# Kernel optimization log

Measured on AMD Instinct MI355X. Metric: run time of the kernel, lower is better.

The kernel has to match this reference:

```python
import jax, jax.numpy as jnp
import numpy as np

B, S, D, H = 2, 2048, 1024, 16
DK = D // H
THETA = 10000.0


def _freqs_cos_sin(dim, seq_len, theta=THETA):
    # matches precompute_freqs_cis: freqs over full d_model, pairs of adjacent dims
    inv = 1.0 / theta ** (np.arange(0, dim, 2)[: dim // 2].astype(np.float32) / dim)
    t = np.arange(seq_len, dtype=np.float32)
    ang = np.outer(t, inv)  # [S, D/2]
    return jnp.asarray(np.cos(ang)), jnp.asarray(np.sin(ang))


def setup_inputs() -> dict:
    key = jax.random.key(0)
    ks = jax.random.split(key, 11)
    sc = 1.0 / np.sqrt(D)
    cos, sin = _freqs_cos_sin(D, S)
    return {
        "query": jax.random.normal(ks[0], (B, S, D), jnp.float32),
        "key": jax.random.normal(ks[1], (B, S, D), jnp.float32),
        "value": jax.random.normal(ks[2], (B, S, D), jnp.float32),
        "wq": jax.random.normal(ks[3], (D, D), jnp.float32) * sc,
        "bq": jnp.zeros((D,), jnp.float32),
        "wk": jax.random.normal(ks[4], (D, D), jnp.float32) * sc,
        "bk": jnp.zeros((D,), jnp.float32),
        "wv": jax.random.normal(ks[5], (D, D), jnp.float32) * sc,
        "bv": jnp.zeros((D,), jnp.float32),
        "wo": jax.random.normal(ks[6], (D, D), jnp.float32) * sc,
        "bo": jnp.zeros((D,), jnp.float32),
        "cos": cos,  # [S, D/2]
        "sin": sin,  # [S, D/2]
    }


def _rope(x, cos, sin):
    # x: [B,S,D]; pairs are adjacent elements along D (view_as_complex semantics)
    xr = x.reshape(*x.shape[:-1], -1, 2)  # [B,S,D/2,2]
    x0, x1 = xr[..., 0], xr[..., 1]
    c, s = cos[None], sin[None]  # broadcast over batch
    o0 = x0 * c - x1 * s
    o1 = x0 * s + x1 * c
    return jnp.stack([o0, o1], axis=-1).reshape(x.shape)


def reference(query, key, value, wq, bq, wk, bk, wv, bv, wo, bo, cos, sin):
    q = query @ wq.T + bq
    k = key @ wk.T + bk
    v = value @ wv.T + bv
    q = _rope(q, cos, sin)
    k = _rope(k, cos, sin)
    # split heads: [B,S,D] -> [B,H,S,DK]
    q = q.reshape(B, S, H, DK).transpose(0, 2, 1, 3)
    k = k.reshape(B, S, H, DK).transpose(0, 2, 1, 3)
    v = v.reshape(B, S, H, DK).transpose(0, 2, 1, 3)
    scores = jnp.einsum("bhqd,bhkd->bhqk", q, k) / jnp.sqrt(jnp.float32(DK))
    attn = jax.nn.softmax(scores, axis=-1)  # dropout is identity in eval
    out = jnp.einsum("bhqk,bhkd->bhqd", attn, v)
    out = out.transpose(0, 2, 1, 3).reshape(B, S, D)
    return out @ wo.T + bo
```

## Files before the change

kernel.cpp:

```cpp
#include <hip/hip_runtime.h>
#include <hip/hip_fp16.h>

typedef _Float16 f16;
using f16x8 = __attribute__((ext_vector_type(8))) _Float16;
using h2 = __attribute__((ext_vector_type(2))) __fp16;
using f32x4 = __attribute__((ext_vector_type(4))) float;
using f32x16 = __attribute__((ext_vector_type(16))) float;

#define LOG2E 1.4426950408889634f

__device__ __forceinline__ void gload16(const void* g, void* l) {
  __builtin_amdgcn_global_load_lds(
      (const __attribute__((address_space(1))) void*)g,
      (__attribute__((address_space(3))) void*)l, 16, 0, 0);
}

__device__ __forceinline__ float b32(h2 x) { return __builtin_bit_cast(float, x); }
__device__ __forceinline__ unsigned u32(h2 x) { return __builtin_bit_cast(unsigned, x); }

__global__ __launch_bounds__(256) void convert_k(
    const float* __restrict__ q, const float* __restrict__ k, const float* __restrict__ v,
    const float* __restrict__ wq, const float* __restrict__ wk,
    const float* __restrict__ wv, const float* __restrict__ wo,
    f16* __restrict__ dst) {
  const size_t SEG = (size_t)4 * 1024 * 1024;
  size_t i = ((size_t)blockIdx.x * 256 + threadIdx.x) * 8;
  const float* src; size_t off;
  if (i < SEG)            { src = q;  off = i; }
  else if (i < 2 * SEG)   { src = k;  off = i - SEG; }
  else if (i < 3 * SEG)   { src = v;  off = i - 2 * SEG; }
  else {
    size_t wi = i - 3 * SEG;
    int s = (int)(wi >> 20);
    src = (s == 0) ? wq : (s == 1) ? wk : (s == 2) ? wv : wo;
    off = wi & ((1u << 20) - 1);
  }
  float4 a = *(const float4*)(src + off);
  float4 b = *(const float4*)(src + off + 4);
  f16x8 o;
  o[0] = (f16)a.x; o[1] = (f16)a.y; o[2] = (f16)a.z; o[3] = (f16)a.w;
  o[4] = (f16)b.x; o[5] = (f16)b.y; o[6] = (f16)b.z; o[7] = (f16)b.w;
  *(f16x8*)(dst + i) = o;
}

template <int QKV>
__global__ __launch_bounds__(256) void gemm_k(
    const f16* __restrict__ Abase, const f16* __restrict__ Wbase,
    const float* __restrict__ b0, const float* __restrict__ b1, const float* __restrict__ b2,
    const float* __restrict__ cosT, const float* __restrict__ sinT,
    f16* __restrict__ qh, f16* __restrict__ kh, f16* __restrict__ vt,
    float* __restrict__ outF) {
  __shared__ f16 As[128 * 32];
  __shared__ f16 Bs[128 * 32];
  int tid = threadIdx.x, wid = tid >> 6, lane = tid & 63;
  int z = QKV ? blockIdx.z : 0;
  const f16* A = Abase + (size_t)z * (4u * 1024 * 1024);
  const f16* W = Wbase + (size_t)z * (1024u * 1024);
  int m0 = blockIdx.y * 128, n0 = blockIdx.x * 128;
  int wr = wid >> 1, wc = wid & 1;
  f32x4 acc[4][4] = {};

  for (int kt = 0; kt < 32; ++kt) {
    int k0 = kt * 32;
    __syncthreads();
#pragma unroll
    for (int p = 0; p < 2; ++p) {
      int row = p * 64 + (tid >> 2);
      int srcslot = (tid & 3) ^ (row & 3);
      gload16(A + (size_t)(m0 + row) * 1024 + k0 + srcslot * 8,
              (void*)(As + p * 2048 + wid * 512));
      gload16(W + (size_t)(n0 + row) * 1024 + k0 + srcslot * 8,
              (void*)(Bs + p * 2048 + wid * 512));
    }
    __syncthreads();
    f16x8 af[4], bf[4];
#pragma unroll
    for (int i = 0; i < 4; ++i) {
      int row = wr * 64 + i * 16 + (lane & 15);
      int slot = (lane >> 4) ^ (row & 3);
      af[i] = *(const f16x8*)(As + row * 32 + slot * 8);
    }
#pragma unroll
    for (int j = 0; j < 4; ++j) {
      int col = wc * 64 + j * 16 + (lane & 15);
      int slot = (lane >> 4) ^ (col & 3);
      bf[j] = *(const f16x8*)(Bs + col * 32 + slot * 8);
    }
#pragma unroll
    for (int i = 0; i < 4; ++i)
#pragma unroll
      for (int j = 0; j < 4; ++j)
        acc[i][j] = __builtin_amdgcn_mfma_f32_16x16x32_f16(af[i], bf[j], acc[i][j], 0, 0, 0);
  }

  const float* bias = QKV ? (z == 0 ? b0 : (z == 1 ? b1 : b2)) : b0;
#pragma unroll
  for (int i = 0; i < 4; ++i) {
#pragma unroll
    for (int j = 0; j < 4; ++j) {
#pragma unroll
      for (int r = 0; r < 4; ++r) {
        int grow = m0 + wr * 64 + i * 16 + ((lane >> 4) << 2) + r;
        int gcol = n0 + wc * 64 + j * 16 + (lane & 15);
        float val = acc[i][j][r] + bias[gcol];
        if (QKV) {
          int s = grow & 2047, bb = grow >> 11;
          int h = gcol >> 6, dk = gcol & 63;
          if (z < 2) {
            float pr = __shfl_xor(val, 1);
            int j2 = gcol >> 1;
            float c = cosT[s * 512 + j2], sn = sinT[s * 512 + j2];
            val = (lane & 1) ? (c * val + sn * pr) : (c * val - sn * pr);
            if (z == 0) val *= 0.125f * LOG2E;
            f16* dst = (z == 0) ? qh : kh;
            dst[(((size_t)bb * 16 + h) * 2048 + s) * 64 + dk] = (f16)val;
          } else {
            vt[(((size_t)bb * 16 + h) * 64 + dk) * 2048 + s] = (f16)val;
          }
        } else {
          outF[(size_t)grow * 1024 + gcol] = val;
        }
      }
    }
  }
}

__global__ __launch_bounds__(256, 4) void flash_k(
    const f16* __restrict__ qh, const f16* __restrict__ kh, const f16* __restrict__ vt,
    f16* __restrict__ op, float2* __restrict__ mlbuf) {
  __shared__ f16 Ks[2][64 * 64];
  __shared__ f16 Vs[2][64 * 64];
  int tid = threadIdx.x, wid = tid >> 6, lane = tid & 63;
  int l31 = lane & 31, hi = lane >> 5;
  int qt = blockIdx.x, h = blockIdx.y, z = blockIdx.z;
  int b = z >> 1, ks = z & 1;
  size_t bh = (size_t)b * 16 + h;
  const f16* qp = qh + bh * (2048 * 64);
  const f16* kp = kh + bh * (2048 * 64) + (size_t)ks * 1024 * 64;
  const f16* vp = vt + bh * (64 * 2048) + ks * 1024;
  int qrow = qt * 128 + wid * 32 + l31;

  f16x8 qf[4];
#pragma unroll
  for (int kk = 0; kk < 4; ++kk)
    qf[kk] = *(const f16x8*)(qp + (size_t)qrow * 64 + kk * 16 + hi * 8);

  int srowA = tid >> 3, srowB = srowA + 32;
  int schA = (tid & 7) ^ (srowA & 7);
  int schB = (tid & 7) ^ (srowB & 7);
  const f16* ksrcA = kp + (size_t)srowA * 64 + schA * 8;
  const f16* ksrcB = kp + (size_t)srowB * 64 + schB * 8;
  const f16* vsrcA = vp + (size_t)srowA * 2048 + schA * 8;
  const f16* vsrcB = vp + (size_t)srowB * 2048 + schB * 8;

  int offr[2][4];
#pragma unroll
  for (int kb = 0; kb < 2; ++kb)
#pragma unroll
    for (int kk = 0; kk < 4; ++kk) {
      int row = kb * 32 + l31;
      offr[kb][kk] = (row * 128 + kk * 32 + hi * 16) ^ ((row & 7) << 4);
    }

  float m_ = -1e30f, l_ = 0.f;
  f32x16 oacc[2] = {};

  gload16(ksrcA, (char*)&Ks[0][0] + tid * 16);
  gload16(ksrcB, (char*)&Ks[0][0] + 4096 + tid * 16);
  gload16(vsrcA, (char*)&Vs[0][0] + tid * 16);
  gload16(vsrcB, (char*)&Vs[0][0] + 4096 + tid * 16);
  __syncthreads();

  int cur = 0;
  for (int kt = 0; kt < 16; ++kt) {
    if (kt + 1 < 16) {
      gload16(ksrcA + (size_t)(kt + 1) * 4096, (char*)&Ks[cur ^ 1][0] + tid * 16);
      gload16(ksrcB + (size_t)(kt + 1) * 4096, (char*)&Ks[cur ^ 1][0] + 4096 + tid * 16);
      gload16(vsrcA + (size_t)(kt + 1) * 64, (char*)&Vs[cur ^ 1][0] + tid * 16);
      gload16(vsrcB + (size_t)(kt + 1) * 64, (char*)&Vs[cur ^ 1][0] + 4096 + tid * 16);
    }

    const char* kbase = (const char*)&Ks[cur][0];
    f32x16 sacc[2] = {};
#pragma unroll
    for (int kb = 0; kb < 2; ++kb)
#pragma unroll
      for (int kk = 0; kk < 4; ++kk) {
        f16x8 af = *(const f16x8*)(kbase + offr[kb][kk]);
        sacc[kb] = __builtin_amdgcn_mfma_f32_32x32x16_f16(af, qf[kk], sacc[kb], 0, 0, 0);
      }

    float t16[16];
#pragma unroll
    for (int i = 0; i < 16; ++i) t16[i] = fmaxf(sacc[0][i], sacc[1][i]);
#pragma unroll
    for (int s = 8; s; s >>= 1)
#pragma unroll
      for (int i = 0; i < s; ++i) t16[i] = fmaxf(t16[i], t16[i + s]);
    float pmax = fmaxf(t16[0], __shfl_xor(t16[0], 32));

    if (!__all(pmax <= m_ + 8.0f)) {
      float mn = fmaxf(m_, pmax);
      float al = __builtin_amdgcn_exp2f(m_ - mn);
      m_ = mn;
      l_ *= al;
#pragma unroll
      for (int mb = 0; mb < 2; ++mb)
#pragma unroll
        for (int i = 0; i < 16; ++i) oacc[mb][i] *= al;
    }

#pragma unroll
    for (int kb = 0; kb < 2; ++kb)
#pragma unroll
      for (int i = 0; i < 16; ++i)
        sacc[kb][i] = __builtin_amdgcn_exp2f(sacc[kb][i] - m_);
#pragma unroll
    for (int i = 0; i < 16; ++i) t16[i] = sacc[0][i] + sacc[1][i];
#pragma unroll
    for (int s = 8; s; s >>= 1)
#pragma unroll
      for (int i = 0; i < s; ++i) t16[i] += t16[i + s];
    l_ += t16[0] + __shfl_xor(t16[0], 32);

    f16x8 pa[4];
#pragma unroll
    for (int kk = 0; kk < 4; ++kk) {
      int kb = kk >> 1, c8 = (kk & 1) * 8;
      float wA = b32(__builtin_amdgcn_cvt_pkrtz(sacc[kb][c8 + 0], sacc[kb][c8 + 1]));
      float wB = b32(__builtin_amdgcn_cvt_pkrtz(sacc[kb][c8 + 2], sacc[kb][c8 + 3]));
      float wC = b32(__builtin_amdgcn_cvt_pkrtz(sacc[kb][c8 + 4], sacc[kb][c8 + 5]));
      float wD = b32(__builtin_amdgcn_cvt_pkrtz(sacc[kb][c8 + 6], sacc[kb][c8 + 7]));
      float oA = __shfl_xor(wA, 32), oB = __shfl_xor(wB, 32);
      float oC = __shfl_xor(wC, 32), oD = __shfl_xor(wD, 32);
      float4 ff;
      ff.x = hi ? oC : wA;
      ff.y = hi ? oD : wB;
      ff.z = hi ? wC : oA;
      ff.w = hi ? wD : oB;
      pa[kk] = __builtin_bit_cast(f16x8, ff);
    }

    const char* vbase = (const char*)&Vs[cur][0];
#pragma unroll
    for (int kk = 0; kk < 4; ++kk)
#pragma unroll
      for (int mb = 0; mb < 2; ++mb) {
        f16x8 av = *(const f16x8*)(vbase + offr[mb][kk]);
        oacc[mb] = __builtin_amdgcn_mfma_f32_32x32x16_f16(av, pa[kk], oacc[mb], 0, 0, 0);
      }

    __syncthreads();
    cur ^= 1;
  }

  float inv = 1.f / l_;
  f16* orow = op + (((size_t)z * 16 + h) * 2048 + qrow) * 64;
#pragma unroll
  for (int mb = 0; mb < 2; ++mb)
#pragma unroll
    for (int g = 0; g < 4; ++g) {
      uint2 st;
      st.x = u32(__builtin_amdgcn_cvt_pkrtz(oacc[mb][4 * g + 0] * inv, oacc[mb][4 * g + 1] * inv));
      st.y = u32(__builtin_amdgcn_cvt_pkrtz(oacc[mb][4 * g + 2] * inv, oacc[mb][4 * g + 3] * inv));
      *(uint2*)(orow + mb * 32 + g * 8 + hi * 4) = st;
    }
  if (hi == 0)
    mlbuf[((size_t)z * 16 + h) * 2048 + qrow] = make_float2(m_, l_);
}

__global__ __launch_bounds__(256) void combine_k(
    const f16* __restrict__ op, const float2* __restrict__ ml, f16* __restrict__ attnout) {
  int t = blockIdx.x * 256 + threadIdx.x;
  int row = t >> 3, c8 = t & 7;
  int b = row >> 15, h = (row >> 11) & 15, qrow = row & 2047;
  size_t i0 = ((size_t)(b * 2 + 0) * 16 + h) * 2048 + qrow;
  size_t i1 = ((size_t)(b * 2 + 1) * 16 + h) * 2048 + qrow;
  float2 a = ml[i0], c = ml[i1];
  float M = fmaxf(a.x, c.x);
  float w1 = a.y * __builtin_amdgcn_exp2f(a.x - M);
  float w2 = c.y * __builtin_amdgcn_exp2f(c.x - M);
  float inv = 1.f / (w1 + w2);
  w1 *= inv; w2 *= inv;
  f16x8 o1 = *(const f16x8*)(op + i0 * 64 + c8 * 8);
  f16x8 o2 = *(const f16x8*)(op + i1 * 64 + c8 * 8);
  f16x8 o;
#pragma unroll
  for (int e = 0; e < 8; ++e)
    o[e] = (f16)(w1 * (float)o1[e] + w2 * (float)o2[e]);
  *(f16x8*)(attnout + ((size_t)b * 2048 + qrow) * 1024 + h * 64 + c8 * 8) = o;
}

extern "C" void kernel_launch(void* const* d_in, const int* in_sizes, int n_in,
                              void* d_out, int out_size, void* d_ws, size_t ws_size,
                              hipStream_t stream) {
  (void)in_sizes; (void)n_in; (void)out_size; (void)ws_size;
  const float* query = (const float*)d_in[0];
  const float* key   = (const float*)d_in[1];
  const float* value = (const float*)d_in[2];
  const float* wq = (const float*)d_in[3];
  const float* bq = (const float*)d_in[4];
  const float* wk = (const float*)d_in[5];
  const float* bk = (const float*)d_in[6];
  const float* wv = (const float*)d_in[7];
  const float* bv = (const float*)d_in[8];
  const float* wo = (const float*)d_in[9];
  const float* bo = (const float*)d_in[10];
  const float* cosT = (const float*)d_in[11];
  const float* sinT = (const float*)d_in[12];
  float* out = (float*)d_out;
  f16* ws = (f16*)d_ws;
  const size_t SEG = (size_t)4 * 1024 * 1024;
  f16* Xh = ws;
  f16* Wh = ws + 3 * SEG;
  f16* qh = ws + 16u * 1024 * 1024;
  f16* kh = qh + SEG;
  f16* vt = kh + SEG;
  f16* attnout = ws;
  f16* op = ws + SEG;
  float2* mlb = (float2*)(ws + 12u * 1024 * 1024);

  convert_k<<<8192, 256, 0, stream>>>(query, key, value, wq, wk, wv, wo, ws);
  gemm_k<1><<<dim3(8, 32, 3), 256, 0, stream>>>(Xh, Wh, bq, bk, bv, cosT, sinT,
                                                qh, kh, vt, nullptr);
  flash_k<<<dim3(16, 16, 4), 256, 0, stream>>>(qh, kh, vt, op, mlb);
  combine_k<<<2048, 256, 0, stream>>>(op, mlb, attnout);
  gemm_k<0><<<dim3(8, 32, 1), 256, 0, stream>>>(attnout, Wh + 3u * 1024 * 1024, bo,
                                                nullptr, nullptr, nullptr, nullptr,
                                                nullptr, nullptr, nullptr, out);
}
```

Measured before the change: 162.1 us.

## Double-buffer GEMM LDS tiles to overlap global loads with MFMA

Doubles the shared-memory A and B tiles in the projection GEMM and prefetches the next K-slice into the alternate buffer while MFMAs consume the current one. This cuts the per-iteration barrier pair to a single barrier. It also precomputes the source pointers and swizzled LDS read offsets outside the loop. The cost is twice the LDS per block, which may lower occupancy. Correctness depends on the single barrier ordering the async global_load_lds writes against the reads of the other buffer.

```diff
diff --git a/kernel.cpp b/kernel.cpp
--- a/kernel.cpp
+++ b/kernel.cpp
@@ -50,8 +50,8 @@
     const float* __restrict__ cosT, const float* __restrict__ sinT,
     f16* __restrict__ qh, f16* __restrict__ kh, f16* __restrict__ vt,
     float* __restrict__ outF) {
-  __shared__ f16 As[128 * 32];
-  __shared__ f16 Bs[128 * 32];
+  __shared__ f16 As[2][128 * 32];
+  __shared__ f16 Bs[2][128 * 32];
   int tid = threadIdx.x, wid = tid >> 6, lane = tid & 63;
   int z = QKV ? blockIdx.z : 0;
   const f16* A = Abase + (size_t)z * (4u * 1024 * 1024);
@@ -60,37 +60,50 @@
   int wr = wid >> 1, wc = wid & 1;
   f32x4 acc[4][4] = {};
 
+  int srow = tid >> 2;
+  int sslot = (tid & 3) ^ (srow & 3);
+  const f16* asrc0 = A + (size_t)(m0 + srow) * 1024 + sslot * 8;
+  const f16* asrc1 = A + (size_t)(m0 + 64 + srow) * 1024 + sslot * 8;
+  const f16* bsrc0 = W + (size_t)(n0 + srow) * 1024 + sslot * 8;
+  const f16* bsrc1 = W + (size_t)(n0 + 64 + srow) * 1024 + sslot * 8;
+
+  int aoff[4], boff[4];
+#pragma unroll
+  for (int i = 0; i < 4; ++i) {
+    int row = wr * 64 + i * 16 + (lane & 15);
+    aoff[i] = row * 32 + (((lane >> 4) ^ (row & 3)) * 8);
+    int col = wc * 64 + i * 16 + (lane & 15);
+    boff[i] = col * 32 + (((lane >> 4) ^ (col & 3)) * 8);
+  }
+
+  gload16(asrc0, (void*)(&As[0][0] + wid * 512));
+  gload16(asrc1, (void*)(&As[0][0] + 2048 + wid * 512));
+  gload16(bsrc0, (void*)(&Bs[0][0] + wid * 512));
+  gload16(bsrc1, (void*)(&Bs[0][0] + 2048 + wid * 512));
+  __syncthreads();
+
+  int cur = 0;
   for (int kt = 0; kt < 32; ++kt) {
-    int k0 = kt * 32;
-    __syncthreads();
-#pragma unroll
-    for (int p = 0; p < 2; ++p) {
-      int row = p * 64 + (tid >> 2);
-      int srcslot = (tid & 3) ^ (row & 3);
-      gload16(A + (size_t)(m0 + row) * 1024 + k0 + srcslot * 8,
-              (void*)(As + p * 2048 + wid * 512));
-      gload16(W + (size_t)(n0 + row) * 1024 + k0 + srcslot * 8,
-              (void*)(Bs + p * 2048 + wid * 512));
-    }
-    __syncthreads();
+    if (kt + 1 < 32) {
+      int k0 = (kt + 1) * 32;
+      gload16(asrc0 + k0, (void*)(&As[cur ^ 1][0] + wid * 512));
+      gload16(asrc1 + k0, (void*)(&As[cur ^ 1][0] + 2048 + wid * 512));
+      gload16(bsrc0 + k0, (void*)(&Bs[cur ^ 1][0] + wid * 512));
+      gload16(bsrc1 + k0, (void*)(&Bs[cur ^ 1][0] + 2048 + wid * 512));
+    }
     f16x8 af[4], bf[4];
 #pragma unroll
     for (int i = 0; i < 4; ++i) {
-      int row = wr * 64 + i * 16 + (lane & 15);
-      int slot = (lane >> 4) ^ (row & 3);
-      af[i] = *(const f16x8*)(As + row * 32 + slot * 8);
-    }
-#pragma unroll
-    for (int j = 0; j < 4; ++j) {
-      int col = wc * 64 + j * 16 + (lane & 15);
-      int slot = (lane >> 4) ^ (col & 3);
-      bf[j] = *(const f16x8*)(Bs + col * 32 + slot * 8);
+      af[i] = *(const f16x8*)(&As[cur][0] + aoff[i]);
+      bf[i] = *(const f16x8*)(&Bs[cur][0] + boff[i]);
     }
 #pragma unroll
     for (int i = 0; i < 4; ++i)
 #pragma unroll
       for (int j = 0; j < 4; ++j)
         acc[i][j] = __builtin_amdgcn_mfma_f32_16x16x32_f16(af[i], bf[j], acc[i][j], 0, 0, 0);
+    __syncthreads();
+    cur ^= 1;
   }
 
   const float* bias = QKV ? (z == 0 ? b0 : (z == 1 ? b1 : b2)) : b0;
```

New measurement: 170.4 us. 5.2% more time.
